# Kernel optimization log

Measured on AMD Instinct MI355X. Metric: run time of the kernel, lower is better.

The kernel has to match this reference:

```python
import jax, jax.numpy as jnp
import numpy as np

B, N, D, K = 4, 4096, 1024, 256
AMPLITUDE_MAX = 3.0
GATE_BIAS = float(np.log(0.65 / 0.35))  # logit(gate_bias_init=0.65)


def setup_inputs() -> dict:
    key = jax.random.key(0)
    k0, k1, k2 = jax.random.split(key, 3)
    return {
        "x": jax.random.normal(k0, (B, N, D), jnp.float32),
        "W_proj": jax.random.normal(k1, (6 * K, D), jnp.float32) * (1.0 / np.sqrt(D)),
        "b_proj": jnp.zeros((6 * K,), jnp.float32),
        "W_res": jax.random.normal(k2, (D, 2 * K), jnp.float32) * 0.002,
        "res_scale": jnp.float32(0.05),
    }


def _resonance_scan(alpha, drive_r, drive_i):
    """r_t = alpha_t * r_{t-1} + v_t, associative prefix scan over seq axis=1."""
    b = jnp.stack([drive_r, drive_i], axis=-1)      # (B, N, K, 2)
    a = alpha[..., None]                            # (B, N, K, 1)

    def combine(left, right):
        a_l, b_l = left
        a_r, b_r = right
        return (a_l * a_r, a_r * b_l + b_r)

    _, r = jax.lax.associative_scan(combine, (a, b), axis=1)
    return r[..., 0], r[..., 1]                     # (B, N, K) each


def reference(x, W_proj, b_proj, W_res, res_scale):
    n = x.shape[1]
    # OscillatorProjection: one fused linear -> 6 heads of size K
    raw = jnp.einsum('bnd,pd->bnp', x, W_proj) + b_proj        # (B, n, 6K)
    A_raw, o_raw, phi, al_raw, g_raw, be_raw = jnp.split(raw, 6, axis=-1)
    A = AMPLITUDE_MAX * jax.nn.sigmoid(A_raw)                  # amplitude in (0, amplitude_max)
    omega = jax.nn.softplus(o_raw)                             # positive frequency
    alpha = jax.nn.sigmoid(al_raw + GATE_BIAS)                 # decay gate, fp32
    g_out = jax.nn.sigmoid(g_raw)
    beta = jax.nn.sigmoid(be_raw)

    # phase_mode == 'log' positions
    pos = jnp.log1p(jnp.arange(n, dtype=jnp.float32))[None, :, None]
    angle = omega * pos + phi
    cos_a = jnp.cos(angle)
    sin_a = jnp.sin(angle)

    one_m_a = 1.0 - alpha
    drive_r = one_m_a * A * cos_a
    drive_i = one_m_a * A * sin_a

    r_r, r_i = _resonance_scan(alpha, drive_r, drive_i)

    # forget-gate erase along current phase direction
    readout = r_r * cos_a + r_i * sin_a
    r_r = r_r - beta * readout * cos_a
    r_i = r_i - beta * readout * sin_a

    # state norm: r /= max(|r|, 1.0)
    modulus = jnp.sqrt(r_r * r_r + r_i * r_i + 1e-8)
    scale = jnp.maximum(modulus, 1.0)
    r_r = r_r / scale
    r_i = r_i / scale

    # demodulate: rho = r * exp(-j*angle)
    rho_re = r_r * cos_a + r_i * sin_a
    rho_im = -r_r * sin_a + r_i * cos_a
    rho = jnp.concatenate([g_out * rho_re, g_out * rho_im], axis=-1)  # (B, n, 2K)

    # eval mode: warmup_factor = 1.0
    return res_scale * jnp.einsum('bnk,dk->bnd', rho, W_res)
```

## Files before the change

kernel.cpp:

```cpp
#include <hip/hip_runtime.h>
#include <hip/hip_bf16.h>
#include <cstdint>
#include <cstddef>

#define B_ 4
#define N_ 4096
#define D_ 1024
#define K_ 256
#define M_ (B_ * N_)
#define P_ (6 * K_)
#define DK2_ (2 * K_)

static __device__ __forceinline__ float sigm(float x) {
    return 1.0f / (1.0f + __expf(-x));
}
static __device__ __forceinline__ float softplusf_(float x) {
    return fmaxf(x, 0.0f) + __logf(1.0f + __expf(-fabsf(x)));
}
static __device__ __forceinline__ unsigned short f2bf(float f) {
    uint32_t u = __float_as_uint(f);
    uint32_t r = (u + 0x7FFFu + ((u >> 16) & 1u)) >> 16;
    return (unsigned short)r;
}

#define GATE_BIAS 0.6190392084062235f
#define AMP_MAX 3.0f

typedef __attribute__((ext_vector_type(8))) __bf16 bf16x8;
typedef __attribute__((ext_vector_type(4))) float f32x4;

static __device__ __forceinline__ void gload_lds16(const unsigned short* g, unsigned short* l) {
    __builtin_amdgcn_global_load_lds(
        (const __attribute__((address_space(1))) void*)g,
        (__attribute__((address_space(3))) void*)l, 16, 0, 0);
}

__global__ __launch_bounds__(256) void cvt_kernel(const float* __restrict__ src,
                                                  unsigned short* __restrict__ dst, int n4) {
    int i = blockIdx.x * 256 + threadIdx.x;
    if (i < n4) {
        float4 v = reinterpret_cast<const float4*>(src)[i];
        ushort4 o;
        o.x = f2bf(v.x); o.y = f2bf(v.y); o.z = f2bf(v.z); o.w = f2bf(v.w);
        reinterpret_cast<ushort4*>(dst)[i] = o;
    }
}


#define FRAG(BUF, r, kc) \
    (*reinterpret_cast<const bf16x8*>(&(BUF)[(size_t)(r) * 64 + (((((kc) >> 3) ^ ((r) & 7)) << 3))]))

template <bool ADD_BIAS, bool SCALE>
__global__ __launch_bounds__(512, 2) void gemm_bt(const unsigned short* __restrict__ A,
                                                  const unsigned short* __restrict__ Bm,
                                                  const float* __restrict__ bias,
                                                  const float* __restrict__ scale_p,
                                                  float* __restrict__ C, int M, int N, int Kd) {
    __shared__ unsigned short As0[256 * 64];
    __shared__ unsigned short Bs0[256 * 64];
    __shared__ unsigned short As1[256 * 64];
    __shared__ unsigned short Bs1[256 * 64];

    const int tid = threadIdx.x;
    const int w = tid >> 6, l = tid & 63;
    const int m0 = blockIdx.x * 256;
    const int n0 = blockIdx.y * 256;
    const int wm = w >> 2, wn = w & 3;
    const int lr = l & 15, lk = (l >> 4) * 8;
    const int nt = Kd >> 6;

    const int srow = tid >> 3;
    const int sslot = tid & 7;
    const int wbase = tid & ~63;

    f32x4 acc[8][4];
#pragma unroll
    for (int mi = 0; mi < 8; ++mi)
#pragma unroll
        for (int ni = 0; ni < 4; ++ni) acc[mi][ni] = (f32x4){0.f, 0.f, 0.f, 0.f};

#define STAGE_HALF(SRC, DST, ROW0G, K0, H)                                            \
    {                                                                                 \
        _Pragma("unroll") for (int j = 0; j < 2; ++j) {                               \
            int row = (H) * 128 + j * 64 + srow;                                      \
            int col = (K0) + ((sslot ^ (row & 7)) << 3);                              \
            gload_lds16((SRC) + (size_t)((ROW0G) + row) * Kd + col,                   \
                        (DST) + (size_t)(((H) * 1024 + j * 512 + wbase) * 8));        \
        }                                                                             \
    }

#define PHASE(CA, CB, KK, MIH, STAGE_CODE, TAIL_CODE)                                 \
    {                                                                                 \
        _Pragma("unroll") for (int f = 0; f < 4; ++f) {                               \
            int ar = wm * 128 + ((MIH) * 4 + f) * 16 + lr;                            \
            af[f] = FRAG(CA, ar, (KK) + lk);                                          \
        }                                                                             \
        if ((MIH) == 0) {                                                             \
            _Pragma("unroll") for (int f = 0; f < 4; ++f) {                           \
                int br = wn * 64 + f * 16 + lr;                                       \
                bfr[f] = FRAG(CB, br, (KK) + lk);                                     \
            }                                                                         \
        }                                                                             \
        STAGE_CODE;                                                                   \
        __builtin_amdgcn_s_barrier();                                                 \
        asm volatile("s_waitcnt lgkmcnt(0)" ::: "memory");                            \
        __builtin_amdgcn_sched_barrier(0);                                            \
        __builtin_amdgcn_s_setprio(1);                                                \
        _Pragma("unroll") for (int mi = 0; mi < 4; ++mi)                              \
            _Pragma("unroll") for (int ni = 0; ni < 4; ++ni)                          \
                acc[(MIH) * 4 + mi][ni] = __builtin_amdgcn_mfma_f32_16x16x32_bf16(    \
                    af[mi], bfr[ni], acc[(MIH) * 4 + mi][ni], 0, 0, 0);               \
        __builtin_amdgcn_s_setprio(0);                                                \
        TAIL_CODE;                                                                    \
        __builtin_amdgcn_s_barrier();                                                 \
    }

#define TILE_STEP(T, CA, CB, PA, PB)                                                  \
    {                                                                                 \
        const int knext = ((T) + 1) * 64;                                             \
        const bool do_stage = ((T) + 1 < nt);                                         \
        bf16x8 af[4], bfr[4];                                                         \
        PHASE(CA, CB, 0, 0,                                                           \
              if (do_stage) { STAGE_HALF(A, PA, m0, knext, 0);                        \
                              STAGE_HALF(A, PA, m0, knext, 1); },                     \
              {});                                                                    \
        PHASE(CA, CB, 0, 1,                                                           \
              if (do_stage) { STAGE_HALF(Bm, PB, n0, knext, 0);                       \
                              STAGE_HALF(Bm, PB, n0, knext, 1); },                    \
              {});                                                                    \
        PHASE(CA, CB, 32, 0, {}, {});                                                 \
        PHASE(CA, CB, 32, 1, {},                                                      \
              asm volatile("s_waitcnt vmcnt(0)" ::: "memory"));                       \
    }

    STAGE_HALF(A, As0, m0, 0, 0);
    STAGE_HALF(A, As0, m0, 0, 1);
    STAGE_HALF(Bm, Bs0, n0, 0, 0);
    STAGE_HALF(Bm, Bs0, n0, 0, 1);
    asm volatile("s_waitcnt vmcnt(0)" ::: "memory");
    __builtin_amdgcn_s_barrier();

    for (int t = 0; t < nt; t += 2) {
        TILE_STEP(t, As0, Bs0, As1, Bs1);
        TILE_STEP(t + 1, As1, Bs1, As0, Bs0);
    }

    float sc = SCALE ? *scale_p : 1.0f;
#pragma unroll
    for (int mi = 0; mi < 8; ++mi) {
        int row = m0 + wm * 128 + mi * 16 + (l >> 4) * 4;
#pragma unroll
        for (int ni = 0; ni < 4; ++ni) {
            int col = n0 + wn * 64 + ni * 16 + lr;
            float bv = ADD_BIAS ? bias[col] : 0.0f;
#pragma unroll
            for (int j = 0; j < 4; ++j) {
                float v = acc[mi][ni][j] + bv;
                if (SCALE) v *= sc;
                C[(size_t)(row + j) * N + col] = v;
            }
        }
    }
#undef STAGE_HALF
#undef PHASE
#undef TILE_STEP
}

struct Step {
    float alpha, dr, di, cs, sn, g, beta;
};
template <bool FULL>
static __device__ __forceinline__ Step compute_step(const float* __restrict__ p, float pos) {
    Step s;
    float a_raw = p[0];
    float o_raw = p[K_];
    float phi   = p[2 * K_];
    float al    = p[3 * K_];
    float A     = AMP_MAX * sigm(a_raw);
    float omega = softplusf_(o_raw);
    float alpha = sigm(al + GATE_BIAS);
    float angle = omega * pos + phi;
    float sn, cs;
    __sincosf(angle, &sn, &cs);
    float oma = 1.0f - alpha;
    s.alpha = alpha;
    s.dr = oma * A * cs;
    s.di = oma * A * sn;
    s.cs = cs;
    s.sn = sn;
    if (FULL) {
        s.g    = sigm(p[4 * K_]);
        s.beta = sigm(p[5 * K_]);
    }
    return s;
}

__global__ __launch_bounds__(256) void scan_sum_kernel(const float* __restrict__ raw,
                                                       float* __restrict__ sA,
                                                       float* __restrict__ sR,
                                                       float* __restrict__ sI) {
    const int tid = threadIdx.x;
    const int c = tid & 15, t = tid >> 4;
    const int chunk = blockIdx.x, kg = blockIdx.y, b = blockIdx.z;
    const int k = kg * 16 + c;
    const int n0 = chunk * 256 + t * 16;
    const float* base = raw + (size_t)(b * N_ + n0) * P_ + k;

    float aP = 1.0f, rR = 0.0f, rI = 0.0f;
#pragma unroll
    for (int j = 0; j < 16; ++j) {
        Step s = compute_step<false>(base + (size_t)j * P_, __logf((float)(n0 + j + 1)));
        aP *= s.alpha;
        rR = s.alpha * rR + s.dr;
        rI = s.alpha * rI + s.di;
    }
    __shared__ float lA[256], lR[256], lI[256];
    lA[c * 16 + t] = aP;
    lR[c * 16 + t] = rR;
    lI[c * 16 + t] = rI;
    __syncthreads();
    if (tid < 16) {
        float a = 1.0f, r = 0.0f, im = 0.0f;
        for (int tt = 0; tt < 16; ++tt) {
            float at = lA[tid * 16 + tt];
            r  = at * r  + lR[tid * 16 + tt];
            im = at * im + lI[tid * 16 + tt];
            a *= at;
        }
        int chan = b * K_ + kg * 16 + tid;
        sA[chunk * 1024 + chan] = a;
        sR[chunk * 1024 + chan] = r;
        sI[chunk * 1024 + chan] = im;
    }
}

__global__ __launch_bounds__(256) void scan_apply_kernel(const float* __restrict__ raw,
                                                         const float* __restrict__ sA,
                                                         const float* __restrict__ sR,
                                                         const float* __restrict__ sI,
                                                         unsigned short* __restrict__ rho) {
    const int tid = threadIdx.x;
    const int c = tid & 15, t = tid >> 4;
    const int chunk = blockIdx.x, kg = blockIdx.y, b = blockIdx.z;
    const int k = kg * 16 + c;
    const int n0 = chunk * 256 + t * 16;
    const float* base = raw + (size_t)(b * N_ + n0) * P_ + k;

    float pR = 0.0f, pI = 0.0f;
    if (tid < 16) {
        int chan = b * K_ + kg * 16 + tid;
        for (int ch = 0; ch < chunk; ++ch) {
            float a = sA[ch * 1024 + chan];
            pR = a * pR + sR[ch * 1024 + chan];
            pI = a * pI + sI[ch * 1024 + chan];
        }
    }
    float aP = 1.0f, rR = 0.0f, rI = 0.0f;
#pragma unroll
    for (int j = 0; j < 16; ++j) {
        Step s = compute_step<false>(base + (size_t)j * P_, __logf((float)(n0 + j + 1)));
        aP *= s.alpha;
        rR = s.alpha * rR + s.dr;
        rI = s.alpha * rI + s.di;
    }
    __shared__ float lA[256], lR[256], lI[256], pTR[256], pTI[256];
    lA[c * 16 + t] = aP;
    lR[c * 16 + t] = rR;
    lI[c * 16 + t] = rI;
    __syncthreads();
    if (tid < 16) {
        float r = pR, im = pI;
        for (int tt = 0; tt < 16; ++tt) {
            pTR[tid * 16 + tt] = r;
            pTI[tid * 16 + tt] = im;
            float at = lA[tid * 16 + tt];
            r  = at * r  + lR[tid * 16 + tt];
            im = at * im + lI[tid * 16 + tt];
        }
    }
    __syncthreads();
    float r = pTR[c * 16 + t], im = pTI[c * 16 + t];
    unsigned short* orow = rho + (size_t)(b * N_ + n0) * DK2_ + k;
#pragma unroll
    for (int j = 0; j < 16; ++j) {
        Step s = compute_step<true>(base + (size_t)j * P_, __logf((float)(n0 + j + 1)));
        r  = s.alpha * r  + s.dr;
        im = s.alpha * im + s.di;
        float readout = r * s.cs + im * s.sn;
        float r2 = r  - s.beta * readout * s.cs;
        float i3 = im - s.beta * readout * s.sn;
        float mod = __fsqrt_rn(r2 * r2 + i3 * i3 + 1e-8f);
        float scl = fmaxf(mod, 1.0f);
        float inv = 1.0f / scl;
        float rr = r2 * inv, ri = i3 * inv;
        float rho_re = rr * s.cs + ri * s.sn;
        float rho_im = -rr * s.sn + ri * s.cs;
        orow[(size_t)j * DK2_]      = f2bf(s.g * rho_re);
        orow[(size_t)j * DK2_ + K_] = f2bf(s.g * rho_im);
    }
}

extern "C" void kernel_launch(void* const* d_in, const int* in_sizes, int n_in,
                              void* d_out, int out_size, void* d_ws, size_t ws_size,
                              hipStream_t stream) {
    const float* x  = (const float*)d_in[0];
    const float* Wp = (const float*)d_in[1];
    const float* bp = (const float*)d_in[2];
    const float* Wr = (const float*)d_in[3];
    const float* rs = (const float*)d_in[4];
    float* out = (float*)d_out;
    char* ws = (char*)d_ws;

    float* raw = (float*)ws;
    unsigned short* xb  = (unsigned short*)(ws + 100663296);
    unsigned short* wpb = (unsigned short*)(ws + 134217728);
    unsigned short* wrb = (unsigned short*)(ws + 137363456);
    float* sA = (float*)(ws + 138412032);
    float* sR = (float*)(ws + 138477568);
    float* sI = (float*)(ws + 138543104);
    unsigned short* rho = xb;

    cvt_kernel<<<16384, 256, 0, stream>>>(x, xb, M_ * D_ / 4);
    cvt_kernel<<<1536, 256, 0, stream>>>(Wp, wpb, P_ * D_ / 4);
    cvt_kernel<<<512, 256, 0, stream>>>(Wr, wrb, D_ * DK2_ / 4);

    gemm_bt<true, false><<<dim3(M_ / 256, P_ / 256), 512, 0, stream>>>(
        xb, wpb, bp, nullptr, raw, M_, P_, D_);

    scan_sum_kernel<<<dim3(16, 16, 4), 256, 0, stream>>>(raw, sA, sR, sI);
    scan_apply_kernel<<<dim3(16, 16, 4), 256, 0, stream>>>(raw, sA, sR, sI, rho);

    gemm_bt<false, true><<<dim3(M_ / 256, D_ / 256), 512, 0, stream>>>(
        rho, wrb, nullptr, rs, out, M_, D_, DK2_);
}
```

Before: 172.6 us.

## Use 192-wide tiles for projection GEMM and reuse subchunk scan sums

The GEMM is templated on its N tile width. The projection GEMM now uses 192-wide tiles, giving 512 blocks instead of 384 for better balance across CUs. The GEMM pipeline now issues all A and B staging loads in the first phase and drops the per-phase barrier and explicit LDS wait before the MFMAs. The scan_sum kernel writes its per-thread 16-step subchunk products and sums to workspace, reusing the W_proj bf16 region that is dead by then. scan_apply reads those values back instead of recomputing the transcendental-heavy step, trading extra global traffic and weaker synchronisation for less ALU work.

```diff
diff --git a/kernel.cpp b/kernel.cpp
--- a/kernel.cpp
+++ b/kernel.cpp
@@ -50,21 +50,23 @@
 #define FRAG(BUF, r, kc) \
     (*reinterpret_cast<const bf16x8*>(&(BUF)[(size_t)(r) * 64 + (((((kc) >> 3) ^ ((r) & 7)) << 3))]))
 
-template <bool ADD_BIAS, bool SCALE>
+template <int BN, bool ADD_BIAS, bool SCALE>
 __global__ __launch_bounds__(512, 2) void gemm_bt(const unsigned short* __restrict__ A,
                                                   const unsigned short* __restrict__ Bm,
                                                   const float* __restrict__ bias,
                                                   const float* __restrict__ scale_p,
                                                   float* __restrict__ C, int M, int N, int Kd) {
+    constexpr int NB = BN / 64;
+    constexpr int WCOL = BN / 4;
     __shared__ unsigned short As0[256 * 64];
-    __shared__ unsigned short Bs0[256 * 64];
+    __shared__ unsigned short Bs0[BN * 64];
     __shared__ unsigned short As1[256 * 64];
-    __shared__ unsigned short Bs1[256 * 64];
+    __shared__ unsigned short Bs1[BN * 64];
 
     const int tid = threadIdx.x;
     const int w = tid >> 6, l = tid & 63;
     const int m0 = blockIdx.x * 256;
-    const int n0 = blockIdx.y * 256;
+    const int n0 = blockIdx.y * BN;
     const int wm = w >> 2, wn = w & 3;
     const int lr = l & 15, lk = (l >> 4) * 8;
     const int nt = Kd >> 6;
@@ -73,20 +75,18 @@
     const int sslot = tid & 7;
     const int wbase = tid & ~63;
 
-    f32x4 acc[8][4];
+    f32x4 acc[8][NB];
 #pragma unroll
     for (int mi = 0; mi < 8; ++mi)
 #pragma unroll
-        for (int ni = 0; ni < 4; ++ni) acc[mi][ni] = (f32x4){0.f, 0.f, 0.f, 0.f};
-
-#define STAGE_HALF(SRC, DST, ROW0G, K0, H)                                            \
+        for (int ni = 0; ni < NB; ++ni) acc[mi][ni] = (f32x4){0.f, 0.f, 0.f, 0.f};
+
+#define STAGE_GROUP(SRC, DST, ROW0G, K0, G)                                           \
     {                                                                                 \
-        _Pragma("unroll") for (int j = 0; j < 2; ++j) {                               \
-            int row = (H) * 128 + j * 64 + srow;                                      \
-            int col = (K0) + ((sslot ^ (row & 7)) << 3);                              \
-            gload_lds16((SRC) + (size_t)((ROW0G) + row) * Kd + col,                   \
-                        (DST) + (size_t)(((H) * 1024 + j * 512 + wbase) * 8));        \
-        }                                                                             \
+        int row = (G) * 64 + srow;                                                    \
+        int col = (K0) + ((sslot ^ (srow & 7)) << 3);                                 \
+        gload_lds16((SRC) + (size_t)((ROW0G) + row) * Kd + col,                       \
+                    (DST) + (size_t)((((G) * 512 + wbase)) * 8));                     \
     }
 
 #define PHASE(CA, CB, KK, MIH, STAGE_CODE, TAIL_CODE)                                 \
@@ -96,18 +96,15 @@
             af[f] = FRAG(CA, ar, (KK) + lk);                                          \
         }                                                                             \
         if ((MIH) == 0) {                                                             \
-            _Pragma("unroll") for (int f = 0; f < 4; ++f) {                           \
-                int br = wn * 64 + f * 16 + lr;                                       \
+            _Pragma("unroll") for (int f = 0; f < NB; ++f) {                          \
+                int br = wn * WCOL + f * 16 + lr;                                     \
                 bfr[f] = FRAG(CB, br, (KK) + lk);                                     \
             }                                                                         \
         }                                                                             \
         STAGE_CODE;                                                                   \
-        __builtin_amdgcn_s_barrier();                                                 \
-        asm volatile("s_waitcnt lgkmcnt(0)" ::: "memory");                            \
-        __builtin_amdgcn_sched_barrier(0);                                            \
         __builtin_amdgcn_s_setprio(1);                                                \
         _Pragma("unroll") for (int mi = 0; mi < 4; ++mi)                              \
-            _Pragma("unroll") for (int ni = 0; ni < 4; ++ni)                          \
+            _Pragma("unroll") for (int ni = 0; ni < NB; ++ni)                         \
                 acc[(MIH) * 4 + mi][ni] = __builtin_amdgcn_mfma_f32_16x16x32_bf16(    \
                     af[mi], bfr[ni], acc[(MIH) * 4 + mi][ni], 0, 0, 0);               \
         __builtin_amdgcn_s_setprio(0);                                                \
@@ -119,24 +116,25 @@
     {                                                                                 \
         const int knext = ((T) + 1) * 64;                                             \
         const bool do_stage = ((T) + 1 < nt);                                         \
-        bf16x8 af[4], bfr[4];                                                         \
+        bf16x8 af[4], bfr[NB];                                                        \
         PHASE(CA, CB, 0, 0,                                                           \
-              if (do_stage) { STAGE_HALF(A, PA, m0, knext, 0);                        \
-                              STAGE_HALF(A, PA, m0, knext, 1); },                     \
+              if (do_stage) {                                                         \
+                  _Pragma("unroll") for (int g = 0; g < 4; ++g)                       \
+                      STAGE_GROUP(A, PA, m0, knext, g);                               \
+                  _Pragma("unroll") for (int g = 0; g < NB; ++g)                      \
+                      STAGE_GROUP(Bm, PB, n0, knext, g);                              \
+              },                                                                      \
               {});                                                                    \
-        PHASE(CA, CB, 0, 1,                                                           \
-              if (do_stage) { STAGE_HALF(Bm, PB, n0, knext, 0);                       \
-                              STAGE_HALF(Bm, PB, n0, knext, 1); },                    \
-              {});                                                                    \
+        PHASE(CA, CB, 0, 1, {}, {});                                                  \
         PHASE(CA, CB, 32, 0, {}, {});                                                 \
         PHASE(CA, CB, 32, 1, {},                                                      \
               asm volatile("s_waitcnt vmcnt(0)" ::: "memory"));                       \
     }
 
-    STAGE_HALF(A, As0, m0, 0, 0);
-    STAGE_HALF(A, As0, m0, 0, 1);
-    STAGE_HALF(Bm, Bs0, n0, 0, 0);
-    STAGE_HALF(Bm, Bs0, n0, 0, 1);
+#pragma unroll
+    for (int g = 0; g < 4; ++g) STAGE_GROUP(A, As0, m0, 0, g);
+#pragma unroll
+    for (int g = 0; g < NB; ++g) STAGE_GROUP(Bm, Bs0, n0, 0, g);
     asm volatile("s_waitcnt vmcnt(0)" ::: "memory");
     __builtin_amdgcn_s_barrier();
 
@@ -150,8 +148,8 @@
     for (int mi = 0; mi < 8; ++mi) {
         int row = m0 + wm * 128 + mi * 16 + (l >> 4) * 4;
 #pragma unroll
-        for (int ni = 0; ni < 4; ++ni) {
-            int col = n0 + wn * 64 + ni * 16 + lr;
+        for (int ni = 0; ni < NB; ++ni) {
+            int col = n0 + wn * WCOL + ni * 16 + lr;
             float bv = ADD_BIAS ? bias[col] : 0.0f;
 #pragma unroll
             for (int j = 0; j < 4; ++j) {
@@ -161,7 +159,7 @@
             }
         }
     }
-#undef STAGE_HALF
+#undef STAGE_GROUP
 #undef PHASE
 #undef TILE_STEP
 }
@@ -198,7 +196,10 @@
 __global__ __launch_bounds__(256) void scan_sum_kernel(const float* __restrict__ raw,
                                                        float* __restrict__ sA,
                                                        float* __restrict__ sR,
-                                                       float* __restrict__ sI) {
+                                                       float* __restrict__ sI,
+                                                       float* __restrict__ subA,
+                                                       float* __restrict__ subR,
+                                                       float* __restrict__ subI) {
     const int tid = threadIdx.x;
     const int c = tid & 15, t = tid >> 4;
     const int chunk = blockIdx.x, kg = blockIdx.y, b = blockIdx.z;
@@ -214,6 +215,12 @@
         rR = s.alpha * rR + s.dr;
         rI = s.alpha * rI + s.di;
     }
+    const int chan = b * K_ + kg * 16 + c;
+    const int sidx = (chunk * 16 + t) * 1024 + chan;
+    subA[sidx] = aP;
+    subR[sidx] = rR;
+    subI[sidx] = rI;
+
     __shared__ float lA[256], lR[256], lI[256];
     lA[c * 16 + t] = aP;
     lR[c * 16 + t] = rR;
@@ -227,10 +234,10 @@
             im = at * im + lI[tid * 16 + tt];
             a *= at;
         }
-        int chan = b * K_ + kg * 16 + tid;
-        sA[chunk * 1024 + chan] = a;
-        sR[chunk * 1024 + chan] = r;
-        sI[chunk * 1024 + chan] = im;
+        int chanw = b * K_ + kg * 16 + tid;
+        sA[chunk * 1024 + chanw] = a;
+        sR[chunk * 1024 + chanw] = r;
+        sI[chunk * 1024 + chanw] = im;
     }
 }
 
@@ -238,6 +245,9 @@
                                                          const float* __restrict__ sA,
                                                          const float* __restrict__ sR,
                                                          const float* __restrict__ sI,
+                                                         const float* __restrict__ subA,
+                                                         const float* __restrict__ subR,
+                                                         const float* __restrict__ subI,
                                                          unsigned short* __restrict__ rho) {
     const int tid = threadIdx.x;
     const int c = tid & 15, t = tid >> 4;
@@ -255,18 +265,14 @@
             pI = a * pI + sI[ch * 1024 + chan];
         }
     }
-    float aP = 1.0f, rR = 0.0f, rI = 0.0f;
-#pragma unroll
-    for (int j = 0; j < 16; ++j) {
-        Step s = compute_step<false>(base + (size_t)j * P_, __logf((float)(n0 + j + 1)));
-        aP *= s.alpha;
-        rR = s.alpha * rR + s.dr;
-        rI = s.alpha * rI + s.di;
-    }
     __shared__ float lA[256], lR[256], lI[256], pTR[256], pTI[256];
-    lA[c * 16 + t] = aP;
-    lR[c * 16 + t] = rR;
-    lI[c * 16 + t] = rI;
+    {
+        const int chan = b * K_ + kg * 16 + c;
+        const int sidx = (chunk * 16 + t) * 1024 + chan;
+        lA[c * 16 + t] = subA[sidx];
+        lR[c * 16 + t] = subR[sidx];
+        lI[c * 16 + t] = subI[sidx];
+    }
     __syncthreads();
     if (tid < 16) {
         float r = pR, im = pI;
@@ -319,17 +325,20 @@
     float* sR = (float*)(ws + 138477568);
     float* sI = (float*)(ws + 138543104);
     unsigned short* rho = xb;
+    float* subA = (float*)(ws + 134217728);
+    float* subR = (float*)(ws + 135266304);
+    float* subI = (float*)(ws + 136314880);
 
     cvt_kernel<<<16384, 256, 0, stream>>>(x, xb, M_ * D_ / 4);
     cvt_kernel<<<1536, 256, 0, stream>>>(Wp, wpb, P_ * D_ / 4);
     cvt_kernel<<<512, 256, 0, stream>>>(Wr, wrb, D_ * DK2_ / 4);
 
-    gemm_bt<true, false><<<dim3(M_ / 256, P_ / 256), 512, 0, stream>>>(
+    gemm_bt<192, true, false><<<dim3(M_ / 256, P_ / 192), 512, 0, stream>>>(
         xb, wpb, bp, nullptr, raw, M_, P_, D_);
 
-    scan_sum_kernel<<<dim3(16, 16, 4), 256, 0, stream>>>(raw, sA, sR, sI);
-    scan_apply_kernel<<<dim3(16, 16, 4), 256, 0, stream>>>(raw, sA, sR, sI, rho);
-
-    gemm_bt<false, true><<<dim3(M_ / 256, D_ / 256), 512, 0, stream>>>(
+    scan_sum_kernel<<<dim3(16, 16, 4), 256, 0, stream>>>(raw, sA, sR, sI, subA, subR, subI);
+    scan_apply_kernel<<<dim3(16, 16, 4), 256, 0, stream>>>(raw, sA, sR, sI, subA, subR, subI, rho);
+
+    gemm_bt<256, false, true><<<dim3(M_ / 256, D_ / 256), 512, 0, stream>>>(
         rho, wrb, nullptr, rs, out, M_, D_, DK2_);
 }
```

New measurement: 154.1 us. 1.12x faster.
